# Kernel optimization log

Measured on AMD Instinct MI355X. Metric: run time of the kernel, lower is better.

Reference implementation:

```python
import jax, jax.numpy as jnp
import numpy as np

B, S, D_IN, D_H = 4, 2048, 1024, 1024

def setup_inputs() -> dict:
    key = jax.random.key(0)
    kx, kq, kk, kv = jax.random.split(key, 4)
    # nn.Linear default init: U(-1/sqrt(fan_in), 1/sqrt(fan_in)); stored as [out, in]
    bound = 1.0 / np.sqrt(D_IN)
    x = jax.random.normal(kx, (B, S, D_IN), dtype=jnp.float32)
    W_q = jax.random.uniform(kq, (D_H, D_IN), jnp.float32, -bound, bound)
    W_k = jax.random.uniform(kk, (D_H, D_IN), jnp.float32, -bound, bound)
    W_v = jax.random.uniform(kv, (D_H, D_IN), jnp.float32, -bound, bound)
    return {"x": x, "W_q": W_q, "W_k": W_k, "W_v": W_v}

def reference(x, W_q, W_k, W_v):
    # Q = x @ W_q.T, etc. (nn.Linear with bias=False)
    Q = jnp.einsum('bsd,hd->bsh', x, W_q)
    K = jnp.einsum('bsd,hd->bsh', x, W_k)
    V = jnp.einsum('bsd,hd->bsh', x, W_v)
    # NOTE: original scales by sqrt(Q.shape[1]) == sqrt(seq_len), not sqrt(d)
    scale = 1.0 / jnp.sqrt(jnp.asarray(Q.shape[1], Q.dtype))
    scores = jnp.einsum('bqh,bkh->bqk', Q, K) * scale  # [B,S,S]
    attn = jax.nn.softmax(scores, axis=-1)
    return jnp.einsum('bqk,bkh->bqh', attn, V)
```

## Files before the change

### kernel.cpp

```cpp
#include <hip/hip_runtime.h>

typedef unsigned short ushort_t;
typedef __attribute__((ext_vector_type(8))) __bf16 bf16x8;
typedef __attribute__((ext_vector_type(4))) float floatx4;

__device__ __forceinline__ ushort_t f2bf(float f) {
    unsigned int u = __builtin_bit_cast(unsigned int, f);
    u = (u + 0x7fffu + ((u >> 16) & 1u)) >> 16;
    return (ushort_t)u;
}

__device__ __forceinline__ void async16(const ushort_t* g, ushort_t* l) {
    __builtin_amdgcn_global_load_lds(
        (const __attribute__((address_space(1))) unsigned int*)g,
        (__attribute__((address_space(3))) unsigned int*)l,
        16 , 0 , 0 );
}

__device__ __forceinline__ int xcd_swz(int bid, int cpx) {
    return (bid & 7) * cpx + (bid >> 3);
}

template <int MODE>
__device__ __forceinline__ void frbn_tile(
    const ushort_t* __restrict__ sb, ushort_t* __restrict__ dst,
    const ushort_t* __restrict__ gA, const ushort_t* __restrict__ gB,
    int lda, int ldb, long koff,
    int rb0, int rb1, int ab, int bb,
    floatx4 (&acc)[4][4]) {

    if constexpr (MODE == 2) asm volatile("s_waitcnt vmcnt(0)");
    else                     asm volatile("s_waitcnt vmcnt(6)");
    __builtin_amdgcn_s_barrier();

    if constexpr (MODE == 0) {
        async16(gA + koff,                   dst);
        async16(gA + (long)64 * lda + koff,  dst + 4096);
        async16(gB + koff,                   dst + 8192);
        async16(gB + (long)64 * ldb + koff,  dst + 12288);
        async16(gB + (long)128 * ldb + koff, dst + 16384);
        async16(gB + (long)192 * ldb + koff, dst + 20480);
    }

    bf16x8 aR[4][2], bKc[2][2], bCc[2][2];
#pragma unroll
    for (int fr = 0; fr < 4; fr++) {
        aR[fr][0] = *(const bf16x8*)&sb[ab + fr * 1024 + rb0];
        aR[fr][1] = *(const bf16x8*)&sb[ab + fr * 1024 + rb1];
    }
#pragma unroll
    for (int fc = 0; fc < 2; fc++) {
        bKc[fc][0] = *(const bf16x8*)&sb[bb + fc * 4096 + rb0];
        bKc[fc][1] = *(const bf16x8*)&sb[bb + fc * 4096 + rb1];
    }
    __builtin_amdgcn_s_setprio(1);
#pragma unroll
    for (int fr = 0; fr < 4; fr++)
#pragma unroll
        for (int fc = 0; fc < 2; fc++) {
            acc[fr][fc] = __builtin_amdgcn_mfma_f32_16x16x32_bf16(
                aR[fr][0], bKc[fc][0], acc[fr][fc], 0, 0, 0);
            acc[fr][fc] = __builtin_amdgcn_mfma_f32_16x16x32_bf16(
                aR[fr][1], bKc[fc][1], acc[fr][fc], 0, 0, 0);
        }
    __builtin_amdgcn_s_setprio(0);

#pragma unroll
    for (int fc = 0; fc < 2; fc++) {
        bCc[fc][0] = *(const bf16x8*)&sb[bb + (fc + 2) * 4096 + rb0];
        bCc[fc][1] = *(const bf16x8*)&sb[bb + (fc + 2) * 4096 + rb1];
    }
    __builtin_amdgcn_s_setprio(1);
#pragma unroll
    for (int fr = 0; fr < 4; fr++)
#pragma unroll
        for (int fc = 0; fc < 2; fc++) {
            acc[fr][fc + 2] = __builtin_amdgcn_mfma_f32_16x16x32_bf16(
                aR[fr][0], bCc[fc][0], acc[fr][fc + 2], 0, 0, 0);
            acc[fr][fc + 2] = __builtin_amdgcn_mfma_f32_16x16x32_bf16(
                aR[fr][1], bCc[fc][1], acc[fr][fc + 2], 0, 0, 0);
        }
    __builtin_amdgcn_s_setprio(0);
}

__device__ __forceinline__ void gemm_frbn(
    const ushort_t* __restrict__ A, int lda,
    const ushort_t* __restrict__ B, int ldb,
    int K, int tile_m, int tile_n,
    ushort_t* buf,
    floatx4 (&acc)[4][4]) {

    const int tid  = threadIdx.x;
    const int lane = tid & 63;
    const int wave = tid >> 6;
    const int wm   = wave >> 2;
    const int wn   = wave & 3;
    const int quad = lane >> 4;
    const int l16  = lane & 15;

#pragma unroll
    for (int i = 0; i < 4; i++)
#pragma unroll
        for (int j = 0; j < 4; j++) acc[i][j] = (floatx4){0.f, 0.f, 0.f, 0.f};

    const int srow = tid >> 3;
    const int scg  = (tid & 7) ^ (srow & 7);
    const ushort_t* gA = A + (long)(tile_m + srow) * lda + scg * 8;
    const ushort_t* gB = B + (long)(tile_n + srow) * ldb + scg * 8;
    ushort_t* const ld = buf + tid * 8;

    const int rb0 = l16 * 64 + (((quad)     ^ (l16 & 7)) << 3);
    const int rb1 = l16 * 64 + (((quad + 4) ^ (l16 & 7)) << 3);
    const int ab = wm * 4096;
    const int bb = 8192 + wn * 1024;

    const int nt = K >> 6;

    async16(gA,                        ld);
    async16(gA + (long)64 * lda,       ld + 4096);
    async16(gB,                        ld + 8192);
    async16(gB + (long)64 * ldb,       ld + 12288);
    async16(gB + (long)128 * ldb,      ld + 16384);
    async16(gB + (long)192 * ldb,      ld + 20480);
    async16(gA + 64,                   ld + 24576);
    async16(gA + (long)64 * lda + 64,  ld + 24576 + 4096);
    async16(gB + 64,                   ld + 24576 + 8192);
    async16(gB + (long)64 * ldb + 64,  ld + 24576 + 12288);
    async16(gB + (long)128 * ldb + 64, ld + 24576 + 16384);
    async16(gB + (long)192 * ldb + 64, ld + 24576 + 20480);

    int cur = 0;
    int t = 0;
#pragma unroll 1
    for (; t < nt - 2; ++t) {
        const int nx = (cur == 0) ? 2 : cur - 1;
        frbn_tile<0>(buf + cur * 24576, ld + nx * 24576,
                     gA, gB, lda, ldb, (long)(t + 2) * 64,
                     rb0, rb1, ab, bb, acc);
        cur = (cur == 2) ? 0 : cur + 1;
    }
    frbn_tile<1>(buf + cur * 24576, ld, gA, gB, lda, ldb, 0,
                 rb0, rb1, ab, bb, acc);
    cur = (cur == 2) ? 0 : cur + 1;
    frbn_tile<2>(buf + cur * 24576, ld, gA, gB, lda, ldb, 0,
                 rb0, rb1, ab, bb, acc);
}

__global__ void prep_kernel(const float* __restrict__ x,
                            const float* __restrict__ wq,
                            const float* __restrict__ wk,
                            const float* __restrict__ wv,
                            ushort_t* __restrict__ xb,
                            ushort_t* __restrict__ wvb,
                            ushort_t* __restrict__ wqT,
                            ushort_t* __restrict__ wkT,
                            float* __restrict__ lsum) {
    const int bx = blockIdx.x;
    const int t = threadIdx.x;
    if (bx < 9216) {
        const float* src;
        ushort_t* dst;
        long g;
        if (bx < 8192) { src = x;  dst = xb;  g = ((long)bx * 256 + t) * 4; }
        else           { src = wv; dst = wvb; g = ((long)(bx - 8192) * 256 + t) * 4; }
        float4 v = *(const float4*)(src + g);
        ushort4 o;
        o.x = f2bf(v.x); o.y = f2bf(v.y); o.z = f2bf(v.z); o.w = f2bf(v.w);
        *(ushort4*)(dst + g) = o;
        return;
    }
    if (bx < 9224) {
        int idx = (bx - 9216) * 256 + t;
        ((float4*)lsum)[idx] = (float4){0.f, 0.f, 0.f, 0.f};
        return;
    }
    const int tt = bx - 9224;
    const float* src = (tt >= 256) ? wk : wq;
    ushort_t* dst = (tt >= 256) ? wkT : wqT;
    const int id = tt & 255;
    const int h0 = (id >> 4) * 64, d0 = (id & 15) * 64;
    __shared__ ushort_t tile[64 * 80];
    {
        int i = t >> 2, cg = (t & 3) << 4;
        const float4* p = (const float4*)(src + (long)(h0 + i) * 1024 + d0 + cg);
#pragma unroll
        for (int k = 0; k < 4; k++) {
            float4 v = p[k];
            ushort_t* q = &tile[i * 80 + cg + k * 4];
            q[0] = f2bf(v.x); q[1] = f2bf(v.y); q[2] = f2bf(v.z); q[3] = f2bf(v.w);
        }
    }
    __syncthreads();
    {
        int j = t >> 2, ig = (t & 3) << 4;
        ushort_t tmp[16];
#pragma unroll
        for (int k = 0; k < 16; k++) tmp[k] = tile[(ig + k) * 80 + j];
        ushort_t* o = dst + (long)(d0 + j) * 1024 + h0 + ig;
        *(uint4*)o = ((uint4*)tmp)[0];
        *(uint4*)(o + 8) = ((uint4*)tmp)[1];
    }
}

__global__ __launch_bounds__(512, 2) void gv_kernel(
    const ushort_t* __restrict__ wkT, const ushort_t* __restrict__ wqT,
    const ushort_t* __restrict__ wvb, const ushort_t* __restrict__ xb,
    ushort_t* __restrict__ Gb, ushort_t* __restrict__ VTb) {

    __shared__ __align__(16) ushort_t buf[73728];

    const int lin = xcd_swz(blockIdx.x, 36);
    const ushort_t *A, *B;
    ushort_t* C;
    int ldc, tile_m, tile_n;
    if (lin < 32) {
        A = wkT; B = wqT; C = Gb; ldc = 1024;
        tile_m = (lin >> 2) * 128;
        tile_n = (lin & 3) * 256;
    } else {
        int id = lin - 32;
        A = wvb; B = xb; C = VTb; ldc = 8192;
        tile_m = (id >> 5) * 128;
        tile_n = (id & 31) * 256;
    }

    floatx4 acc[4][4];
    gemm_frbn(A, 1024, B, 1024, 1024, tile_m, tile_n, buf, acc);

    const int lane = threadIdx.x & 63, wave = threadIdx.x >> 6;
    const int wm = wave >> 2, wn = wave & 3, quad = lane >> 4, l16 = lane & 15;
#pragma unroll
    for (int fr = 0; fr < 4; fr++)
#pragma unroll
        for (int r = 0; r < 4; r++) {
            int row = tile_m + wm * 64 + fr * 16 + quad * 4 + r;
#pragma unroll
            for (int fc = 0; fc < 4; fc++) {
                int col = tile_n + fc * 64 + wn * 16 + l16;
                C[(long)row * ldc + col] = f2bf(acc[fr][fc][r]);
            }
        }
}

__global__ __launch_bounds__(512, 2) void y_kernel(
    const ushort_t* __restrict__ xb,
    const ushort_t* __restrict__ Gb,
    ushort_t* __restrict__ Yb) {

    __shared__ __align__(16) ushort_t buf[73728];
    const int lin = xcd_swz(blockIdx.x, 32);
    const int tile_m = (lin >> 2) * 128;
    const int tile_n = (lin & 3) * 256;

    floatx4 acc[4][4];
    gemm_frbn(xb, 1024, Gb, 1024, 1024, tile_m, tile_n, buf, acc);

    const int lane = threadIdx.x & 63, wave = threadIdx.x >> 6;
    const int wm = wave >> 2, wn = wave & 3, quad = lane >> 4, l16 = lane & 15;
#pragma unroll
    for (int fr = 0; fr < 4; fr++)
#pragma unroll
        for (int r = 0; r < 4; r++) {
            int row = tile_m + wm * 64 + fr * 16 + quad * 4 + r;
#pragma unroll
            for (int fc = 0; fc < 4; fc++) {
                int col = tile_n + fc * 64 + wn * 16 + l16;
                Yb[(long)row * 1024 + col] = f2bf(acc[fr][fc][r]);
            }
        }
}

__global__ __launch_bounds__(512, 2) void pexp_kernel(
    const ushort_t* __restrict__ Yb,
    const ushort_t* __restrict__ xb,
    ushort_t* __restrict__ Pb,
    float* __restrict__ lsum) {

    __shared__ __align__(16) ushort_t buf[73728];

    const int lin = xcd_swz(blockIdx.x, 64);
    const int z = lin >> 7;
    const int tile_m = ((lin >> 3) & 15) * 128;
    const int tile_n = (lin & 7) * 256;

    const ushort_t* A = Yb + (long)z * 2097152;
    const ushort_t* B = xb + (long)z * 2097152;
    ushort_t* C = Pb + (long)z * 4194304;
    float* l = lsum + z * 2048;

    floatx4 acc[4][4];
    gemm_frbn(A, 1024, B, 1024, 1024, tile_m, tile_n, buf, acc);

    const float scale = 0.022097086912079608f;
    const int lane = threadIdx.x & 63, wave = threadIdx.x >> 6;
    const int wm = wave >> 2, wn = wave & 3, quad = lane >> 4, l16 = lane & 15;
#pragma unroll
    for (int fr = 0; fr < 4; fr++)
#pragma unroll
        for (int r = 0; r < 4; r++) {
            int row = tile_m + wm * 64 + fr * 16 + quad * 4 + r;
            float psum = 0.f;
#pragma unroll
            for (int fc = 0; fc < 4; fc++) {
                int col = tile_n + fc * 64 + wn * 16 + l16;
                float e = __expf(acc[fr][fc][r] * scale);
                C[(long)row * 2048 + col] = f2bf(e);
                psum += e;
            }
            psum += __shfl_xor(psum, 1, 64);
            psum += __shfl_xor(psum, 2, 64);
            psum += __shfl_xor(psum, 4, 64);
            psum += __shfl_xor(psum, 8, 64);
            if (l16 == 0) atomicAdd(&l[row], psum);
        }
}

__global__ __launch_bounds__(512, 2) void out_kernel(
    const ushort_t* __restrict__ Pb,
    const ushort_t* __restrict__ VTb,
    float* __restrict__ out,
    const float* __restrict__ lsum) {

    __shared__ __align__(16) ushort_t buf[73728];

    const int lin = xcd_swz(blockIdx.x, 32);
    const int z = lin >> 6;
    const int tile_m = ((lin >> 2) & 15) * 128;
    const int tile_n = (lin & 3) * 256;

    const ushort_t* A = Pb + (long)z * 4194304;
    const ushort_t* B = VTb + (long)z * 2048;
    float* C = out + (long)z * 2097152;
    const float* l = lsum + z * 2048;

    floatx4 acc[4][4];
    gemm_frbn(A, 2048, B, 8192, 2048, tile_m, tile_n, buf, acc);

    const int lane = threadIdx.x & 63, wave = threadIdx.x >> 6;
    const int wm = wave >> 2, wn = wave & 3, quad = lane >> 4, l16 = lane & 15;
#pragma unroll
    for (int fr = 0; fr < 4; fr++)
#pragma unroll
        for (int r = 0; r < 4; r++) {
            int row = tile_m + wm * 64 + fr * 16 + quad * 4 + r;
            float li = 1.0f / l[row];
#pragma unroll
            for (int fc = 0; fc < 4; fc++) {
                int col = tile_n + fc * 64 + wn * 16 + l16;
                C[(long)row * 1024 + col] = acc[fr][fc][r] * li;
            }
        }
}

extern "C" void kernel_launch(void* const* d_in, const int* in_sizes, int n_in,
                              void* d_out, int out_size, void* d_ws, size_t ws_size,
                              hipStream_t stream) {
    const float* x  = (const float*)d_in[0];
    const float* wq = (const float*)d_in[1];
    const float* wk = (const float*)d_in[2];
    const float* wv = (const float*)d_in[3];

    ushort_t* xb  = (ushort_t*)d_ws;
    ushort_t* wvb = xb  + 8388608;
    ushort_t* wqT = wvb + 1048576;
    ushort_t* wkT = wqT + 1048576;
    ushort_t* Gb  = wkT + 1048576;
    ushort_t* Yb  = Gb  + 1048576;
    ushort_t* VTb = Yb  + 8388608;
    ushort_t* Pb  = VTb + 8388608;
    float*    lsum = (float*)(Pb + 16777216);
    float*    out  = (float*)d_out;

    prep_kernel<<<9736, 256, 0, stream>>>(x, wq, wk, wv, xb, wvb, wqT, wkT, lsum);
    gv_kernel<<<288, 512, 0, stream>>>(wkT, wqT, wvb, xb, Gb, VTb);
    y_kernel<<<256, 512, 0, stream>>>(xb, Gb, Yb);
    pexp_kernel<<<512, 512, 0, stream>>>(Yb, xb, Pb, lsum);
    out_kernel<<<256, 512, 0, stream>>>(Pb, VTb, out, lsum);
}
```

Measured before the change: 229.1 us.

## Switch GEMMs to 128x128 tiles with 256 threads and K-step 32

Replaces the 128x256 tile, 512-thread, K=64 GEMM core with a 128x128 tile, 4-wave, K=32 core using a smaller triple-buffered LDS footprint, and doubles the grid sizes of all four GEMM kernels. The aim is more blocks across the CUs, higher occupancy (3 blocks per CU) and less LDS per block. In exchange, each K step does less compute per barrier and operand reuse per tile drops.

```diff
diff --git a/kernel.cpp b/kernel.cpp
--- a/kernel.cpp
+++ b/kernel.cpp
@@ -22,68 +22,40 @@
 }
 
 template <int MODE>
-__device__ __forceinline__ void frbn_tile(
+__device__ __forceinline__ void fr128_tile(
     const ushort_t* __restrict__ sb, ushort_t* __restrict__ dst,
     const ushort_t* __restrict__ gA, const ushort_t* __restrict__ gB,
     int lda, int ldb, long koff,
-    int rb0, int rb1, int ab, int bb,
+    int rbA, int rbB,
     floatx4 (&acc)[4][4]) {
 
     if constexpr (MODE == 2) asm volatile("s_waitcnt vmcnt(0)");
-    else                     asm volatile("s_waitcnt vmcnt(6)");
+    else                     asm volatile("s_waitcnt vmcnt(4)");
     __builtin_amdgcn_s_barrier();
 
     if constexpr (MODE == 0) {
-        async16(gA + koff,                   dst);
-        async16(gA + (long)64 * lda + koff,  dst + 4096);
-        async16(gB + koff,                   dst + 8192);
-        async16(gB + (long)64 * ldb + koff,  dst + 12288);
-        async16(gB + (long)128 * ldb + koff, dst + 16384);
-        async16(gB + (long)192 * ldb + koff, dst + 20480);
-    }
-
-    bf16x8 aR[4][2], bKc[2][2], bCc[2][2];
-#pragma unroll
-    for (int fr = 0; fr < 4; fr++) {
-        aR[fr][0] = *(const bf16x8*)&sb[ab + fr * 1024 + rb0];
-        aR[fr][1] = *(const bf16x8*)&sb[ab + fr * 1024 + rb1];
-    }
-#pragma unroll
-    for (int fc = 0; fc < 2; fc++) {
-        bKc[fc][0] = *(const bf16x8*)&sb[bb + fc * 4096 + rb0];
-        bKc[fc][1] = *(const bf16x8*)&sb[bb + fc * 4096 + rb1];
-    }
+        async16(gA + koff,                  dst);
+        async16(gA + (long)64 * lda + koff, dst + 2048);
+        async16(gB + koff,                  dst + 4096);
+        async16(gB + (long)64 * ldb + koff, dst + 6144);
+    }
+
+    bf16x8 af[4], bf[4];
+#pragma unroll
+    for (int fr = 0; fr < 4; fr++) af[fr] = *(const bf16x8*)&sb[rbA + fr * 512];
+#pragma unroll
+    for (int fc = 0; fc < 4; fc++) bf[fc] = *(const bf16x8*)&sb[rbB + fc * 512];
     __builtin_amdgcn_s_setprio(1);
 #pragma unroll
     for (int fr = 0; fr < 4; fr++)
 #pragma unroll
-        for (int fc = 0; fc < 2; fc++) {
+        for (int fc = 0; fc < 4; fc++)
             acc[fr][fc] = __builtin_amdgcn_mfma_f32_16x16x32_bf16(
-                aR[fr][0], bKc[fc][0], acc[fr][fc], 0, 0, 0);
-            acc[fr][fc] = __builtin_amdgcn_mfma_f32_16x16x32_bf16(
-                aR[fr][1], bKc[fc][1], acc[fr][fc], 0, 0, 0);
-        }
+                af[fr], bf[fc], acc[fr][fc], 0, 0, 0);
     __builtin_amdgcn_s_setprio(0);
-
-#pragma unroll
-    for (int fc = 0; fc < 2; fc++) {
-        bCc[fc][0] = *(const bf16x8*)&sb[bb + (fc + 2) * 4096 + rb0];
-        bCc[fc][1] = *(const bf16x8*)&sb[bb + (fc + 2) * 4096 + rb1];
-    }
-    __builtin_amdgcn_s_setprio(1);
-#pragma unroll
-    for (int fr = 0; fr < 4; fr++)
-#pragma unroll
-        for (int fc = 0; fc < 2; fc++) {
-            acc[fr][fc + 2] = __builtin_amdgcn_mfma_f32_16x16x32_bf16(
-                aR[fr][0], bCc[fc][0], acc[fr][fc + 2], 0, 0, 0);
-            acc[fr][fc + 2] = __builtin_amdgcn_mfma_f32_16x16x32_bf16(
-                aR[fr][1], bCc[fc][1], acc[fr][fc + 2], 0, 0, 0);
-        }
-    __builtin_amdgcn_s_setprio(0);
-}
-
-__device__ __forceinline__ void gemm_frbn(
+}
+
+__device__ __forceinline__ void gemm_fr128(
     const ushort_t* __restrict__ A, int lda,
     const ushort_t* __restrict__ B, int ldb,
     int K, int tile_m, int tile_n,
@@ -93,8 +65,7 @@
     const int tid  = threadIdx.x;
     const int lane = tid & 63;
     const int wave = tid >> 6;
-    const int wm   = wave >> 2;
-    const int wn   = wave & 3;
+    const int wm   = wave >> 1, wn = wave & 1;
     const int quad = lane >> 4;
     const int l16  = lane & 15;
 
@@ -103,47 +74,40 @@
 #pragma unroll
         for (int j = 0; j < 4; j++) acc[i][j] = (floatx4){0.f, 0.f, 0.f, 0.f};
 
-    const int srow = tid >> 3;
-    const int scg  = (tid & 7) ^ (srow & 7);
+    const int srow = tid >> 2;
+    const int scg  = (tid & 3) ^ (srow & 3);
     const ushort_t* gA = A + (long)(tile_m + srow) * lda + scg * 8;
     const ushort_t* gB = B + (long)(tile_n + srow) * ldb + scg * 8;
     ushort_t* const ld = buf + tid * 8;
 
-    const int rb0 = l16 * 64 + (((quad)     ^ (l16 & 7)) << 3);
-    const int rb1 = l16 * 64 + (((quad + 4) ^ (l16 & 7)) << 3);
-    const int ab = wm * 4096;
-    const int bb = 8192 + wn * 1024;
-
-    const int nt = K >> 6;
-
-    async16(gA,                        ld);
-    async16(gA + (long)64 * lda,       ld + 4096);
-    async16(gB,                        ld + 8192);
-    async16(gB + (long)64 * ldb,       ld + 12288);
-    async16(gB + (long)128 * ldb,      ld + 16384);
-    async16(gB + (long)192 * ldb,      ld + 20480);
-    async16(gA + 64,                   ld + 24576);
-    async16(gA + (long)64 * lda + 64,  ld + 24576 + 4096);
-    async16(gB + 64,                   ld + 24576 + 8192);
-    async16(gB + (long)64 * ldb + 64,  ld + 24576 + 12288);
-    async16(gB + (long)128 * ldb + 64, ld + 24576 + 16384);
-    async16(gB + (long)192 * ldb + 64, ld + 24576 + 20480);
+    const int sw8 = (quad ^ (l16 & 3)) << 3;
+    const int rbA = (wm * 64 + l16) * 32 + sw8;
+    const int rbB = 4096 + (wn * 64 + l16) * 32 + sw8;
+
+    const int nt = K >> 5;
+
+    async16(gA,                      ld);
+    async16(gA + (long)64 * lda,     ld + 2048);
+    async16(gB,                      ld + 4096);
+    async16(gB + (long)64 * ldb,     ld + 6144);
+    async16(gA + 32,                 ld + 8192);
+    async16(gA + (long)64 * lda + 32, ld + 8192 + 2048);
+    async16(gB + 32,                 ld + 8192 + 4096);
+    async16(gB + (long)64 * ldb + 32, ld + 8192 + 6144);
 
     int cur = 0;
     int t = 0;
 #pragma unroll 1
     for (; t < nt - 2; ++t) {
         const int nx = (cur == 0) ? 2 : cur - 1;
-        frbn_tile<0>(buf + cur * 24576, ld + nx * 24576,
-                     gA, gB, lda, ldb, (long)(t + 2) * 64,
-                     rb0, rb1, ab, bb, acc);
+        fr128_tile<0>(buf + cur * 8192, ld + nx * 8192,
+                      gA, gB, lda, ldb, (long)(t + 2) * 32,
+                      rbA, rbB, acc);
         cur = (cur == 2) ? 0 : cur + 1;
     }
-    frbn_tile<1>(buf + cur * 24576, ld, gA, gB, lda, ldb, 0,
-                 rb0, rb1, ab, bb, acc);
+    fr128_tile<1>(buf + cur * 8192, ld, gA, gB, lda, ldb, 0, rbA, rbB, acc);
     cur = (cur == 2) ? 0 : cur + 1;
-    frbn_tile<2>(buf + cur * 24576, ld, gA, gB, lda, ldb, 0,
-                 rb0, rb1, ab, bb, acc);
+    fr128_tile<2>(buf + cur * 8192, ld, gA, gB, lda, ldb, 0, rbA, rbB, acc);
 }
 
 __global__ void prep_kernel(const float* __restrict__ x,
@@ -202,33 +166,33 @@
     }
 }
 
-__global__ __launch_bounds__(512, 2) void gv_kernel(
+__global__ __launch_bounds__(256, 3) void gv_kernel(
     const ushort_t* __restrict__ wkT, const ushort_t* __restrict__ wqT,
     const ushort_t* __restrict__ wvb, const ushort_t* __restrict__ xb,
     ushort_t* __restrict__ Gb, ushort_t* __restrict__ VTb) {
 
-    __shared__ __align__(16) ushort_t buf[73728];
-
-    const int lin = xcd_swz(blockIdx.x, 36);
+    __shared__ __align__(16) ushort_t buf[24576];
+
+    const int lin = xcd_swz(blockIdx.x, 72);
     const ushort_t *A, *B;
     ushort_t* C;
     int ldc, tile_m, tile_n;
-    if (lin < 32) {
+    if (lin < 64) {
         A = wkT; B = wqT; C = Gb; ldc = 1024;
-        tile_m = (lin >> 2) * 128;
-        tile_n = (lin & 3) * 256;
+        tile_m = (lin >> 3) * 128;
+        tile_n = (lin & 7) * 128;
     } else {
-        int id = lin - 32;
+        int id = lin - 64;
         A = wvb; B = xb; C = VTb; ldc = 8192;
-        tile_m = (id >> 5) * 128;
-        tile_n = (id & 31) * 256;
+        tile_m = (id >> 6) * 128;
+        tile_n = (id & 63) * 128;
     }
 
     floatx4 acc[4][4];
-    gemm_frbn(A, 1024, B, 1024, 1024, tile_m, tile_n, buf, acc);
+    gemm_fr128(A, 1024, B, 1024, 1024, tile_m, tile_n, buf, acc);
 
     const int lane = threadIdx.x & 63, wave = threadIdx.x >> 6;
-    const int wm = wave >> 2, wn = wave & 3, quad = lane >> 4, l16 = lane & 15;
+    const int wm = wave >> 1, wn = wave & 1, quad = lane >> 4, l16 = lane & 15;
 #pragma unroll
     for (int fr = 0; fr < 4; fr++)
 #pragma unroll
@@ -236,27 +200,27 @@
             int row = tile_m + wm * 64 + fr * 16 + quad * 4 + r;
 #pragma unroll
             for (int fc = 0; fc < 4; fc++) {
-                int col = tile_n + fc * 64 + wn * 16 + l16;
+                int col = tile_n + wn * 64 + fc * 16 + l16;
                 C[(long)row * ldc + col] = f2bf(acc[fr][fc][r]);
             }
         }
 }
 
-__global__ __launch_bounds__(512, 2) void y_kernel(
+__global__ __launch_bounds__(256, 3) void y_kernel(
     const ushort_t* __restrict__ xb,
     const ushort_t* __restrict__ Gb,
     ushort_t* __restrict__ Yb) {
 
-    __shared__ __align__(16) ushort_t buf[73728];
-    const int lin = xcd_swz(blockIdx.x, 32);
-    const int tile_m = (lin >> 2) * 128;
-    const int tile_n = (lin & 3) * 256;
+    __shared__ __align__(16) ushort_t buf[24576];
+    const int lin = xcd_swz(blockIdx.x, 64);
+    const int tile_m = (lin >> 3) * 128;
+    const int tile_n = (lin & 7) * 128;
 
     floatx4 acc[4][4];
-    gemm_frbn(xb, 1024, Gb, 1024, 1024, tile_m, tile_n, buf, acc);
+    gemm_fr128(xb, 1024, Gb, 1024, 1024, tile_m, tile_n, buf, acc);
 
     const int lane = threadIdx.x & 63, wave = threadIdx.x >> 6;
-    const int wm = wave >> 2, wn = wave & 3, quad = lane >> 4, l16 = lane & 15;
+    const int wm = wave >> 1, wn = wave & 1, quad = lane >> 4, l16 = lane & 15;
 #pragma unroll
     for (int fr = 0; fr < 4; fr++)
 #pragma unroll
@@ -264,24 +228,24 @@
             int row = tile_m + wm * 64 + fr * 16 + quad * 4 + r;
 #pragma unroll
             for (int fc = 0; fc < 4; fc++) {
-                int col = tile_n + fc * 64 + wn * 16 + l16;
+                int col = tile_n + wn * 64 + fc * 16 + l16;
                 Yb[(long)row * 1024 + col] = f2bf(acc[fr][fc][r]);
             }
         }
 }
 
-__global__ __launch_bounds__(512, 2) void pexp_kernel(
+__global__ __launch_bounds__(256, 3) void pexp_kernel(
     const ushort_t* __restrict__ Yb,
     const ushort_t* __restrict__ xb,
     ushort_t* __restrict__ Pb,
     float* __restrict__ lsum) {
 
-    __shared__ __align__(16) ushort_t buf[73728];
-
-    const int lin = xcd_swz(blockIdx.x, 64);
-    const int z = lin >> 7;
-    const int tile_m = ((lin >> 3) & 15) * 128;
-    const int tile_n = (lin & 7) * 256;
+    __shared__ __align__(16) ushort_t buf[24576];
+
+    const int lin = xcd_swz(blockIdx.x, 128);
+    const int z = lin >> 8;
+    const int tile_m = ((lin >> 4) & 15) * 128;
+    const int tile_n = (lin & 15) * 128;
 
     const ushort_t* A = Yb + (long)z * 2097152;
     const ushort_t* B = xb + (long)z * 2097152;
@@ -289,11 +253,11 @@
     float* l = lsum + z * 2048;
 
     floatx4 acc[4][4];
-    gemm_frbn(A, 1024, B, 1024, 1024, tile_m, tile_n, buf, acc);
+    gemm_fr128(A, 1024, B, 1024, 1024, tile_m, tile_n, buf, acc);
 
     const float scale = 0.022097086912079608f;
     const int lane = threadIdx.x & 63, wave = threadIdx.x >> 6;
-    const int wm = wave >> 2, wn = wave & 3, quad = lane >> 4, l16 = lane & 15;
+    const int wm = wave >> 1, wn = wave & 1, quad = lane >> 4, l16 = lane & 15;
 #pragma unroll
     for (int fr = 0; fr < 4; fr++)
 #pragma unroll
@@ -302,7 +266,7 @@
             float psum = 0.f;
 #pragma unroll
             for (int fc = 0; fc < 4; fc++) {
-                int col = tile_n + fc * 64 + wn * 16 + l16;
+                int col = tile_n + wn * 64 + fc * 16 + l16;
                 float e = __expf(acc[fr][fc][r] * scale);
                 C[(long)row * 2048 + col] = f2bf(e);
                 psum += e;
@@ -315,18 +279,18 @@
         }
 }
 
-__global__ __launch_bounds__(512, 2) void out_kernel(
+__global__ __launch_bounds__(256, 3) void out_kernel(
     const ushort_t* __restrict__ Pb,
     const ushort_t* __restrict__ VTb,
     float* __restrict__ out,
     const float* __restrict__ lsum) {
 
-    __shared__ __align__(16) ushort_t buf[73728];
-
-    const int lin = xcd_swz(blockIdx.x, 32);
-    const int z = lin >> 6;
-    const int tile_m = ((lin >> 2) & 15) * 128;
-    const int tile_n = (lin & 3) * 256;
+    __shared__ __align__(16) ushort_t buf[24576];
+
+    const int lin = xcd_swz(blockIdx.x, 64);
+    const int z = lin >> 7;
+    const int tile_m = ((lin >> 3) & 15) * 128;
+    const int tile_n = (lin & 7) * 128;
 
     const ushort_t* A = Pb + (long)z * 4194304;
     const ushort_t* B = VTb + (long)z * 2048;
@@ -334,10 +298,10 @@
     const float* l = lsum + z * 2048;
 
     floatx4 acc[4][4];
-    gemm_frbn(A, 2048, B, 8192, 2048, tile_m, tile_n, buf, acc);
+    gemm_fr128(A, 2048, B, 8192, 2048, tile_m, tile_n, buf, acc);
 
     const int lane = threadIdx.x & 63, wave = threadIdx.x >> 6;
-    const int wm = wave >> 2, wn = wave & 3, quad = lane >> 4, l16 = lane & 15;
+    const int wm = wave >> 1, wn = wave & 1, quad = lane >> 4, l16 = lane & 15;
 #pragma unroll
     for (int fr = 0; fr < 4; fr++)
 #pragma unroll
@@ -346,7 +310,7 @@
             float li = 1.0f / l[row];
 #pragma unroll
             for (int fc = 0; fc < 4; fc++) {
-                int col = tile_n + fc * 64 + wn * 16 + l16;
+                int col = tile_n + wn * 64 + fc * 16 + l16;
                 C[(long)row * 1024 + col] = acc[fr][fc][r] * li;
             }
         }
@@ -372,8 +336,8 @@
     float*    out  = (float*)d_out;
 
     prep_kernel<<<9736, 256, 0, stream>>>(x, wq, wk, wv, xb, wvb, wqT, wkT, lsum);
-    gv_kernel<<<288, 512, 0, stream>>>(wkT, wqT, wvb, xb, Gb, VTb);
-    y_kernel<<<256, 512, 0, stream>>>(xb, Gb, Yb);
-    pexp_kernel<<<512, 512, 0, stream>>>(Yb, xb, Pb, lsum);
-    out_kernel<<<256, 512, 0, stream>>>(Pb, VTb, out, lsum);
-}
+    gv_kernel<<<576, 256, 0, stream>>>(wkT, wqT, wvb, xb, Gb, VTb);
+    y_kernel<<<512, 256, 0, stream>>>(xb, Gb, Yb);
+    pexp_kernel<<<1024, 256, 0, stream>>>(Yb, xb, Pb, lsum);
+    out_kernel<<<512, 256, 0, stream>>>(Pb, VTb, out, lsum);
+}
```

Measured after the change: 240.0 us. +4.8%, slower.

## Split W_k^T W_q GEMM into split-K pass and separate V^T GEMM

Applied to the files above, without the earlier changes.

The fused gv kernel becomes three launches. The G = Wk^T Wq product is split four ways along K across 128 blocks, each writing fp32 partials into the Pb scratch region, and a small reduction kernel sums the partials and converts them to bf16. The V^T GEMM moves to its own 256-block kernel launched after y_kernel. The aim is to remove the load imbalance of the mixed 288-block grid and to give the y_kernel dependency a shorter critical path. The cost is extra fp32 partial traffic, two more launches, and reuse of the Pb buffer, which is safe only because pexp overwrites it later.

```diff
diff --git a/kernel.cpp b/kernel.cpp
--- a/kernel.cpp
+++ b/kernel.cpp
@@ -202,31 +202,23 @@
     }
 }
 
-__global__ __launch_bounds__(512, 2) void gv_kernel(
+__global__ __launch_bounds__(512, 2) void gvg_kernel(
     const ushort_t* __restrict__ wkT, const ushort_t* __restrict__ wqT,
-    const ushort_t* __restrict__ wvb, const ushort_t* __restrict__ xb,
-    ushort_t* __restrict__ Gb, ushort_t* __restrict__ VTb) {
+    float* __restrict__ Gacc) {
 
     __shared__ __align__(16) ushort_t buf[73728];
 
-    const int lin = xcd_swz(blockIdx.x, 36);
-    const ushort_t *A, *B;
-    ushort_t* C;
-    int ldc, tile_m, tile_n;
-    if (lin < 32) {
-        A = wkT; B = wqT; C = Gb; ldc = 1024;
-        tile_m = (lin >> 2) * 128;
-        tile_n = (lin & 3) * 256;
-    } else {
-        int id = lin - 32;
-        A = wvb; B = xb; C = VTb; ldc = 8192;
-        tile_m = (id >> 5) * 128;
-        tile_n = (id & 31) * 256;
-    }
+    const int lin = xcd_swz(blockIdx.x, 16);
+    const int kpart = lin >> 5;
+    const int t5 = lin & 31;
+    const int tile_m = (t5 >> 2) * 128;
+    const int tile_n = (t5 & 3) * 256;
 
     floatx4 acc[4][4];
-    gemm_frbn(A, 1024, B, 1024, 1024, tile_m, tile_n, buf, acc);
-
+    gemm_frbn(wkT + kpart * 256, 1024, wqT + kpart * 256, 1024, 256,
+              tile_m, tile_n, buf, acc);
+
+    float* Gp = Gacc + (long)kpart * 1048576;
     const int lane = threadIdx.x & 63, wave = threadIdx.x >> 6;
     const int wm = wave >> 2, wn = wave & 3, quad = lane >> 4, l16 = lane & 15;
 #pragma unroll
@@ -237,7 +229,50 @@
 #pragma unroll
             for (int fc = 0; fc < 4; fc++) {
                 int col = tile_n + fc * 64 + wn * 16 + l16;
-                C[(long)row * ldc + col] = f2bf(acc[fr][fc][r]);
+                Gp[(long)row * 1024 + col] = acc[fr][fc][r];
+            }
+        }
+}
+
+__global__ void gsum_kernel(const float* __restrict__ Gacc,
+                            ushort_t* __restrict__ Gb) {
+    const int i = blockIdx.x * 256 + threadIdx.x;
+    float4 a = ((const float4*)(Gacc))[i];
+    float4 b = ((const float4*)(Gacc + 1048576))[i];
+    float4 c = ((const float4*)(Gacc + 2097152))[i];
+    float4 d = ((const float4*)(Gacc + 3145728))[i];
+    ushort4 o;
+    o.x = f2bf(a.x + b.x + c.x + d.x);
+    o.y = f2bf(a.y + b.y + c.y + d.y);
+    o.z = f2bf(a.z + b.z + c.z + d.z);
+    o.w = f2bf(a.w + b.w + c.w + d.w);
+    ((ushort4*)Gb)[i] = o;
+}
+
+__global__ __launch_bounds__(512, 2) void gvvt_kernel(
+    const ushort_t* __restrict__ wvb, const ushort_t* __restrict__ xb,
+    ushort_t* __restrict__ VTb) {
+
+    __shared__ __align__(16) ushort_t buf[73728];
+
+    const int lin = xcd_swz(blockIdx.x, 32);
+    const int tile_m = (lin >> 5) * 128;
+    const int tile_n = (lin & 31) * 256;
+
+    floatx4 acc[4][4];
+    gemm_frbn(wvb, 1024, xb, 1024, 1024, tile_m, tile_n, buf, acc);
+
+    const int lane = threadIdx.x & 63, wave = threadIdx.x >> 6;
+    const int wm = wave >> 2, wn = wave & 3, quad = lane >> 4, l16 = lane & 15;
+#pragma unroll
+    for (int fr = 0; fr < 4; fr++)
+#pragma unroll
+        for (int r = 0; r < 4; r++) {
+            int row = tile_m + wm * 64 + fr * 16 + quad * 4 + r;
+#pragma unroll
+            for (int fc = 0; fc < 4; fc++) {
+                int col = tile_n + fc * 64 + wn * 16 + l16;
+                VTb[(long)row * 8192 + col] = f2bf(acc[fr][fc][r]);
             }
         }
 }
@@ -371,9 +406,13 @@
     float*    lsum = (float*)(Pb + 16777216);
     float*    out  = (float*)d_out;
 
+    float* Gacc = (float*)Pb;
+
     prep_kernel<<<9736, 256, 0, stream>>>(x, wq, wk, wv, xb, wvb, wqT, wkT, lsum);
-    gv_kernel<<<288, 512, 0, stream>>>(wkT, wqT, wvb, xb, Gb, VTb);
+    gvg_kernel<<<128, 512, 0, stream>>>(wkT, wqT, Gacc);
+    gsum_kernel<<<1024, 256, 0, stream>>>(Gacc, Gb);
     y_kernel<<<256, 512, 0, stream>>>(xb, Gb, Yb);
+    gvvt_kernel<<<256, 512, 0, stream>>>(wvb, xb, VTb);
     pexp_kernel<<<512, 512, 0, stream>>>(Yb, xb, Pb, lsum);
     out_kernel<<<256, 512, 0, stream>>>(Pb, VTb, out, lsum);
 }
```

Result: slower. 237.5 us (+3.7%).
